# Kernel optimization log

Measured on AMD Instinct MI355X. Metric: run time of the kernel, lower is better.

## Reference

```python
import jax, jax.numpy as jnp
import numpy as np

B, T, C, H = 8, 2048, 1024, 128

def setup_inputs() -> dict:
    key = jax.random.key(0)
    k1, k2, k3, k4 = jax.random.split(key, 4)
    s = 1.0 / np.sqrt(C)
    return {
        "x": jax.random.normal(k1, (B, T, C), dtype=jnp.float32),
        "Wq": jax.random.normal(k2, (C, H), dtype=jnp.float32) * s,
        "Wk": jax.random.normal(k3, (C, H), dtype=jnp.float32) * s,
        "Wv": jax.random.normal(k4, (C, H), dtype=jnp.float32) * s,
    }

def reference(x, Wq, Wk, Wv):
    # q,k,v: [B,T,H]
    q = jnp.einsum('btc,ch->bth', x, Wq)
    k = jnp.einsum('btc,ch->bth', x, Wk)
    v = jnp.einsum('btc,ch->bth', x, Wv)
    scale = k.shape[-1] ** -0.5
    wei = jnp.einsum('bqh,bkh->bqk', q, k) * scale  # [B,T,T]
    # NOTE: original forward never applies the tril mask -> full bidirectional softmax
    wei = jax.nn.softmax(wei, axis=-1)
    # dropout p=0 (eval): identity
    out = jnp.einsum('bqk,bkh->bqh', wei, v)  # [B,T,H]
    return out
```

## Files before the change

kernel.cpp:

```cpp
#include <hip/hip_runtime.h>

typedef __attribute__((ext_vector_type(4))) float  f32x4;
typedef __attribute__((ext_vector_type(8))) short  s16x8;
typedef __attribute__((ext_vector_type(4))) unsigned int u32x4;
typedef __attribute__((ext_vector_type(4))) unsigned short u16x4;

#define NB 8
#define NT 2048
#define NC 1024
#define NH 128
#define NM (NB * NT)

__device__ __forceinline__ unsigned short f2bf(float f) {
  union { float f; unsigned u; } v; v.f = f;
  unsigned r = v.u + 0x7FFFu + ((v.u >> 16) & 1u);
  return (unsigned short)(r >> 16);
}
__device__ __forceinline__ unsigned pack2(float a, float b) {
  return (unsigned)f2bf(a) | ((unsigned)f2bf(b) << 16);
}
__device__ __forceinline__ f32x4 mfma16(s16x8 a, s16x8 b, f32x4 c) {
  return __builtin_amdgcn_mfma_f32_16x16x32_bf16(a, b, c, 0, 0, 0);
}

__global__ __launch_bounds__(256) void k_prep_w(
    const float* __restrict__ wq, const float* __restrict__ wk,
    const float* __restrict__ wv, unsigned short* __restrict__ wt3) {
  int id = blockIdx.x * 256 + threadIdx.x;
  int w = id >> 17;
  int r = id & 131071;
  int c = r & 1023;
  int h = r >> 10;
  const float* W = (w == 0) ? wq : (w == 1) ? wk : wv;
  float v = W[c * NH + h];
  if (w == 0) v *= 0.08838834764831845f;
  wt3[id] = f2bf(v);
}

__global__ __launch_bounds__(256, 2) void k_qkv(
    const float* __restrict__ x, const unsigned short* __restrict__ wt3,
    unsigned short* __restrict__ qo, unsigned short* __restrict__ ko,
    unsigned short* __restrict__ vo) {
  __shared__ u32x4 xs4[32 * 64 * 2 / 16];
  char* xs = (char*)xs4;
  const int tid = threadIdx.x;
  const int lane = tid & 63;
  const int w = tid >> 6;
  const int m0 = blockIdx.x * 32;

  const int sr = tid >> 3;
  const int scb = (tid & 7) * 16;
  const float* xp = x + (size_t)(m0 + sr) * NC + (tid & 7) * 8;
  const int wb = (sr * 128 + scb) ^ ((sr & 7) << 4);

  const int arow = lane & 15;
  const int aswz = (arow & 7) << 4;
  const int akb = (lane >> 4) * 16;
  const int n0 = w * 96;

  f32x4 acc[2][6] = {};
  f32x4 xa = *(const f32x4*)(xp);
  f32x4 xb = *(const f32x4*)(xp + 4);

  for (int kt = 0; kt < 16; ++kt) {
    __syncthreads();
    u32x4 pk = { pack2(xa.x, xa.y), pack2(xa.z, xa.w),
                 pack2(xb.x, xb.y), pack2(xb.z, xb.w) };
    *(u32x4*)(xs + wb) = pk;
    __syncthreads();
    if (kt < 15) {
      xa = *(const f32x4*)(xp + (kt + 1) * 64);
      xb = *(const f32x4*)(xp + (kt + 1) * 64 + 4);
    }
    #pragma unroll
    for (int ks = 0; ks < 2; ++ks) {
      s16x8 a0 = *(const s16x8*)(xs + (((arow)      * 128 + ks * 64 + akb) ^ aswz));
      s16x8 a1 = *(const s16x8*)(xs + (((arow + 16) * 128 + ks * 64 + akb) ^ aswz));
      const unsigned short* wp = wt3 + (size_t)(n0 + (lane & 15)) * NC
                                 + kt * 64 + ks * 32 + (lane >> 4) * 8;
      #pragma unroll
      for (int nj = 0; nj < 6; ++nj) {
        s16x8 bf = *(const s16x8*)(wp + (size_t)nj * 16 * NC);
        acc[0][nj] = mfma16(a0, bf, acc[0][nj]);
        acc[1][nj] = mfma16(a1, bf, acc[1][nj]);
      }
    }
  }
  const int rl = (lane >> 4) * 4;
  #pragma unroll
  for (int m = 0; m < 2; ++m) {
    #pragma unroll
    for (int nj = 0; nj < 6; ++nj) {
      f32x4 a = acc[m][nj];
      int gcol = n0 + nj * 16 + (lane & 15);
      int gr = m0 + m * 16 + rl;
      int h = gcol & 127;
      if (gcol < 256) {
        unsigned short* dst = (gcol < 128) ? qo : ko;
        dst[(size_t)(gr + 0) * NH + h] = f2bf(a.x);
        dst[(size_t)(gr + 1) * NH + h] = f2bf(a.y);
        dst[(size_t)(gr + 2) * NH + h] = f2bf(a.z);
        dst[(size_t)(gr + 3) * NH + h] = f2bf(a.w);
      } else {
        int bb = gr >> 11, tt = gr & 2047;
        u16x4 pv = { f2bf(a.x), f2bf(a.y), f2bf(a.z), f2bf(a.w) };
        *(u16x4*)(vo + ((size_t)(bb * NH + h) * NT + tt)) = pv;
      }
    }
  }
}

__global__ __launch_bounds__(256) void k_attn(
    const unsigned short* __restrict__ qg, const unsigned short* __restrict__ kg,
    const unsigned short* __restrict__ vg, float* __restrict__ out) {
  __shared__ u32x4 lds4[40 * 1024 / 16];
  char* Ks = (char*)lds4;
  char* Vs = Ks + 16 * 1024;
  char* Ps = Vs + 16 * 1024;
  const int tid = threadIdx.x;
  const int lane = tid & 63;
  const int w = tid >> 6;
  const int b = blockIdx.y;
  const int qr = blockIdx.x * 64 + w * 16;
  const int c15 = lane & 15;
  const int g4 = lane >> 4;

  s16x8 qf[4];
  #pragma unroll
  for (int ks = 0; ks < 4; ++ks)
    qf[ks] = *(const s16x8*)(qg + (size_t)(b * NT + qr + c15) * NH + ks * 32 + g4 * 8);

  float m_run[4], l_run[4];
  #pragma unroll
  for (int r = 0; r < 4; ++r) { m_run[r] = -3.0e38f; l_run[r] = 0.0f; }
  f32x4 acc_o[8] = {};

  const int skr = tid >> 4;
  const unsigned short* kbase = kg + (size_t)b * NT * NH + (tid & 15) * 8;
  const int svh = tid >> 3;
  const unsigned short* vbase = vg + (size_t)(b * NH) * NT + (tid & 7) * 8;

  u32x4 kreg[4], vreg[4];
  #pragma unroll
  for (int i = 0; i < 4; ++i) {
    kreg[i] = *(const u32x4*)(kbase + (size_t)(skr + i * 16) * NH);
    vreg[i] = *(const u32x4*)(vbase + (size_t)(svh + i * 32) * NT);
  }
  auto write_tiles = [&]() {
    #pragma unroll
    for (int i = 0; i < 4; ++i) {
      int r = skr + i * 16;
      *(u32x4*)(Ks + ((r * 256 + (tid & 15) * 16) ^ ((r & 7) << 4))) = kreg[i];
      int h = svh + i * 32;
      *(u32x4*)(Vs + ((h * 128 + (tid & 7) * 16) ^ ((h & 7) << 4))) = vreg[i];
    }
  };
  write_tiles();
  __syncthreads();

  char* pw = Ps + w * 2048;

  for (int kt = 0; kt < 32; ++kt) {
    if (kt < 31) {
      #pragma unroll
      for (int i = 0; i < 4; ++i) {
        kreg[i] = *(const u32x4*)(kbase + (size_t)((kt + 1) * 64 + skr + i * 16) * NH);
        vreg[i] = *(const u32x4*)(vbase + (size_t)(svh + i * 32) * NT + (kt + 1) * 64);
      }
    }
    f32x4 s[4] = {};
    #pragma unroll
    for (int nj = 0; nj < 4; ++nj) {
      int krow = nj * 16 + c15;
      int kswz = (krow & 7) << 4;
      #pragma unroll
      for (int ks = 0; ks < 4; ++ks) {
        s16x8 bf = *(const s16x8*)(Ks + ((krow * 256 + ks * 64 + g4 * 16) ^ kswz));
        s[nj] = mfma16(qf[ks], bf, s[nj]);
      }
    }
    float alpha[4];
    #pragma unroll
    for (int r = 0; r < 4; ++r) {
      float pm = fmaxf(fmaxf(s[0][r], s[1][r]), fmaxf(s[2][r], s[3][r]));
      pm = fmaxf(pm, __shfl_xor(pm, 1));
      pm = fmaxf(pm, __shfl_xor(pm, 2));
      pm = fmaxf(pm, __shfl_xor(pm, 4));
      pm = fmaxf(pm, __shfl_xor(pm, 8));
      float mn = fmaxf(m_run[r], pm);
      alpha[r] = __expf(m_run[r] - mn);
      m_run[r] = mn;
      float e0 = __expf(s[0][r] - mn);
      float e1 = __expf(s[1][r] - mn);
      float e2 = __expf(s[2][r] - mn);
      float e3 = __expf(s[3][r] - mn);
      s[0][r] = e0; s[1][r] = e1; s[2][r] = e2; s[3][r] = e3;
      float ps = e0 + e1 + e2 + e3;
      ps += __shfl_xor(ps, 1);
      ps += __shfl_xor(ps, 2);
      ps += __shfl_xor(ps, 4);
      ps += __shfl_xor(ps, 8);
      l_run[r] = l_run[r] * alpha[r] + ps;
    }
    #pragma unroll
    for (int hj = 0; hj < 8; ++hj) {
      acc_o[hj][0] *= alpha[0]; acc_o[hj][1] *= alpha[1];
      acc_o[hj][2] *= alpha[2]; acc_o[hj][3] *= alpha[3];
    }
    #pragma unroll
    for (int nj = 0; nj < 4; ++nj) {
      int colb = (nj * 16 + c15) * 2;
      #pragma unroll
      for (int r = 0; r < 4; ++r) {
        int row = g4 * 4 + r;
        *(unsigned short*)(pw + ((row * 128 + colb) ^ ((row & 7) << 4))) = f2bf(s[nj][r]);
      }
    }
    #pragma unroll
    for (int ks2 = 0; ks2 < 2; ++ks2) {
      s16x8 pa = *(const s16x8*)(pw + ((c15 * 128 + ks2 * 64 + g4 * 16) ^ ((c15 & 7) << 4)));
      #pragma unroll
      for (int hj = 0; hj < 8; ++hj) {
        int vrow = hj * 16 + c15;
        s16x8 bv = *(const s16x8*)(Vs + ((vrow * 128 + ks2 * 64 + g4 * 16) ^ ((vrow & 7) << 4)));
        acc_o[hj] = mfma16(pa, bv, acc_o[hj]);
      }
    }
    __syncthreads();
    if (kt < 31) write_tiles();
    __syncthreads();
  }
  float inv[4];
  #pragma unroll
  for (int r = 0; r < 4; ++r) inv[r] = 1.0f / l_run[r];
  #pragma unroll
  for (int hj = 0; hj < 8; ++hj) {
    int h = hj * 16 + c15;
    #pragma unroll
    for (int r = 0; r < 4; ++r) {
      int t = qr + g4 * 4 + r;
      out[(size_t)(b * NT + t) * NH + h] = acc_o[hj][r] * inv[r];
    }
  }
}

extern "C" void kernel_launch(void* const* d_in, const int* in_sizes, int n_in,
                              void* d_out, int out_size, void* d_ws, size_t ws_size,
                              hipStream_t stream) {
  const float* x  = (const float*)d_in[0];
  const float* wq = (const float*)d_in[1];
  const float* wk = (const float*)d_in[2];
  const float* wv = (const float*)d_in[3];
  unsigned short* ws  = (unsigned short*)d_ws;
  unsigned short* qb  = ws;
  unsigned short* kb  = ws + (size_t)2 * 1024 * 1024;
  unsigned short* vb  = ws + (size_t)4 * 1024 * 1024;
  unsigned short* wt3 = ws + (size_t)6 * 1024 * 1024;

  k_prep_w<<<dim3(1536), dim3(256), 0, stream>>>(wq, wk, wv, wt3);
  k_qkv<<<dim3(NM / 32), dim3(256), 0, stream>>>(x, wt3, qb, kb, vb);
  k_attn<<<dim3(NT / 64, NB), dim3(256), 0, stream>>>(qb, kb, vb, (float*)d_out);
}
```

Before: 219.0 us.

## Split attention KV across two wave groups, double-buffer tiles, tile weight transpose

The attention kernel now runs 512 threads per block. Two groups of four waves each process half of the key/value sequence, using double-buffered K/V tiles in LDS (144 KB) so each iteration needs one barrier instead of two. The two partial softmax states are merged through LDS at the end. The row-sum shuffle reduction is deferred to after the loop, and s_setprio wraps the MFMA sections. The QKV projection also moves to 64-row, 512-thread blocks with double-buffered x staging, and the weight transpose now goes through an LDS tile for coalesced reads and writes. The large LDS footprint limits occupancy to one block per CU, and the merge step adds an epilogue.

```diff
diff --git a/kernel.cpp b/kernel.cpp
--- a/kernel.cpp
+++ b/kernel.cpp
@@ -26,56 +26,71 @@
 __global__ __launch_bounds__(256) void k_prep_w(
     const float* __restrict__ wq, const float* __restrict__ wk,
     const float* __restrict__ wv, unsigned short* __restrict__ wt3) {
-  int id = blockIdx.x * 256 + threadIdx.x;
-  int w = id >> 17;
-  int r = id & 131071;
-  int c = r & 1023;
-  int h = r >> 10;
+  __shared__ float ts[64][65];
+  const int tid = threadIdx.x;
+  const int w = blockIdx.x >> 5;
+  const int rem = blockIdx.x & 31;
+  const int c0 = (rem >> 1) * 64;
+  const int h0 = (rem & 1) * 64;
   const float* W = (w == 0) ? wq : (w == 1) ? wk : wv;
-  float v = W[c * NH + h];
-  if (w == 0) v *= 0.08838834764831845f;
-  wt3[id] = f2bf(v);
-}
-
-__global__ __launch_bounds__(256, 2) void k_qkv(
+  const int hl = tid & 63, ci = tid >> 6;
+  #pragma unroll
+  for (int i = 0; i < 16; ++i) {
+    int cl = i * 4 + ci;
+    ts[cl][hl] = W[(size_t)(c0 + cl) * NH + h0 + hl];
+  }
+  __syncthreads();
+  const int cl2 = tid & 63, hi2 = tid >> 6;
+  #pragma unroll
+  for (int j = 0; j < 16; ++j) {
+    int hl2 = j * 4 + hi2;
+    float v = ts[cl2][hl2];
+    if (w == 0) v *= 0.08838834764831845f;
+    wt3[(size_t)w * 131072 + (size_t)(h0 + hl2) * NC + c0 + cl2] = f2bf(v);
+  }
+}
+
+__global__ __launch_bounds__(512) void k_qkv(
     const float* __restrict__ x, const unsigned short* __restrict__ wt3,
     unsigned short* __restrict__ qo, unsigned short* __restrict__ ko,
     unsigned short* __restrict__ vo) {
-  __shared__ u32x4 xs4[32 * 64 * 2 / 16];
+  __shared__ u32x4 xs4[2 * 64 * 128 / 16];
   char* xs = (char*)xs4;
   const int tid = threadIdx.x;
   const int lane = tid & 63;
   const int w = tid >> 6;
-  const int m0 = blockIdx.x * 32;
+  const int m0 = blockIdx.x * 64;
 
   const int sr = tid >> 3;
-  const int scb = (tid & 7) * 16;
   const float* xp = x + (size_t)(m0 + sr) * NC + (tid & 7) * 8;
-  const int wb = (sr * 128 + scb) ^ ((sr & 7) << 4);
-
-  const int arow = lane & 15;
-  const int aswz = (arow & 7) << 4;
+  const int wb = (sr * 128 + (tid & 7) * 16) ^ ((sr & 7) << 4);
+
+  const int mg = w >> 2;
+  const int n0 = (w & 3) * 96;
+  const int arow0 = mg * 32 + (lane & 15);
+  const int aswz = (arow0 & 7) << 4;
   const int akb = (lane >> 4) * 16;
-  const int n0 = w * 96;
 
   f32x4 acc[2][6] = {};
   f32x4 xa = *(const f32x4*)(xp);
   f32x4 xb = *(const f32x4*)(xp + 4);
-
-  for (int kt = 0; kt < 16; ++kt) {
-    __syncthreads();
+  {
     u32x4 pk = { pack2(xa.x, xa.y), pack2(xa.z, xa.w),
                  pack2(xb.x, xb.y), pack2(xb.z, xb.w) };
     *(u32x4*)(xs + wb) = pk;
-    __syncthreads();
+  }
+  __syncthreads();
+
+  for (int kt = 0; kt < 16; ++kt) {
     if (kt < 15) {
       xa = *(const f32x4*)(xp + (kt + 1) * 64);
       xb = *(const f32x4*)(xp + (kt + 1) * 64 + 4);
     }
+    char* cb = xs + (kt & 1) * 8192;
     #pragma unroll
     for (int ks = 0; ks < 2; ++ks) {
-      s16x8 a0 = *(const s16x8*)(xs + (((arow)      * 128 + ks * 64 + akb) ^ aswz));
-      s16x8 a1 = *(const s16x8*)(xs + (((arow + 16) * 128 + ks * 64 + akb) ^ aswz));
+      s16x8 a0 = *(const s16x8*)(cb + (((arow0)      * 128 + ks * 64 + akb) ^ aswz));
+      s16x8 a1 = *(const s16x8*)(cb + (((arow0 + 16) * 128 + ks * 64 + akb) ^ aswz));
       const unsigned short* wp = wt3 + (size_t)(n0 + (lane & 15)) * NC
                                  + kt * 64 + ks * 32 + (lane >> 4) * 8;
       #pragma unroll
@@ -85,6 +100,12 @@
         acc[1][nj] = mfma16(a1, bf, acc[1][nj]);
       }
     }
+    if (kt < 15) {
+      u32x4 pk = { pack2(xa.x, xa.y), pack2(xa.z, xa.w),
+                   pack2(xb.x, xb.y), pack2(xb.z, xb.w) };
+      *(u32x4*)(xs + ((kt + 1) & 1) * 8192 + wb) = pk;
+    }
+    __syncthreads();
   }
   const int rl = (lane >> 4) * 4;
   #pragma unroll
@@ -93,7 +114,7 @@
     for (int nj = 0; nj < 6; ++nj) {
       f32x4 a = acc[m][nj];
       int gcol = n0 + nj * 16 + (lane & 15);
-      int gr = m0 + m * 16 + rl;
+      int gr = m0 + mg * 32 + m * 16 + rl;
       int h = gcol & 127;
       if (gcol < 256) {
         unsigned short* dst = (gcol < 128) ? qo : ko;
@@ -110,35 +131,41 @@
   }
 }
 
-__global__ __launch_bounds__(256) void k_attn(
+__global__ __launch_bounds__(512) void k_attn(
     const unsigned short* __restrict__ qg, const unsigned short* __restrict__ kg,
     const unsigned short* __restrict__ vg, float* __restrict__ out) {
-  __shared__ u32x4 lds4[40 * 1024 / 16];
-  char* Ks = (char*)lds4;
-  char* Vs = Ks + 16 * 1024;
-  char* Ps = Vs + 16 * 1024;
+  __shared__ u32x4 lds4[147456 / 16];
+  char* L = (char*)lds4;
   const int tid = threadIdx.x;
   const int lane = tid & 63;
   const int w = tid >> 6;
+  const int grp = w >> 2;
+  const int wq = w & 3;
+  const int gt = tid & 255;
   const int b = blockIdx.y;
-  const int qr = blockIdx.x * 64 + w * 16;
+  const int qr = blockIdx.x * 64 + wq * 16;
   const int c15 = lane & 15;
   const int g4 = lane >> 4;
+  const int kv0 = grp * 1024;
+
+  char* Kb0 = L + grp * 65536;
+  char* Vb0 = L + grp * 65536 + 32768;
+  char* pw  = L + 131072 + w * 2048;
 
   s16x8 qf[4];
   #pragma unroll
   for (int ks = 0; ks < 4; ++ks)
     qf[ks] = *(const s16x8*)(qg + (size_t)(b * NT + qr + c15) * NH + ks * 32 + g4 * 8);
 
-  float m_run[4], l_run[4];
-  #pragma unroll
-  for (int r = 0; r < 4; ++r) { m_run[r] = -3.0e38f; l_run[r] = 0.0f; }
+  float m_run[4], lsum[4];
+  #pragma unroll
+  for (int r = 0; r < 4; ++r) { m_run[r] = -3.0e38f; lsum[r] = 0.0f; }
   f32x4 acc_o[8] = {};
 
-  const int skr = tid >> 4;
-  const unsigned short* kbase = kg + (size_t)b * NT * NH + (tid & 15) * 8;
-  const int svh = tid >> 3;
-  const unsigned short* vbase = vg + (size_t)(b * NH) * NT + (tid & 7) * 8;
+  const int skr = gt >> 4;
+  const unsigned short* kbase = kg + (size_t)(b * NT + kv0) * NH + (gt & 15) * 8;
+  const int svh = gt >> 3;
+  const unsigned short* vbase = vg + (size_t)(b * NH) * NT + kv0 + (gt & 7) * 8;
 
   u32x4 kreg[4], vreg[4];
   #pragma unroll
@@ -146,22 +173,22 @@
     kreg[i] = *(const u32x4*)(kbase + (size_t)(skr + i * 16) * NH);
     vreg[i] = *(const u32x4*)(vbase + (size_t)(svh + i * 32) * NT);
   }
-  auto write_tiles = [&]() {
+  auto write_tiles = [&](char* Kd, char* Vd) {
     #pragma unroll
     for (int i = 0; i < 4; ++i) {
       int r = skr + i * 16;
-      *(u32x4*)(Ks + ((r * 256 + (tid & 15) * 16) ^ ((r & 7) << 4))) = kreg[i];
+      *(u32x4*)(Kd + ((r * 256 + (gt & 15) * 16) ^ ((r & 7) << 4))) = kreg[i];
       int h = svh + i * 32;
-      *(u32x4*)(Vs + ((h * 128 + (tid & 7) * 16) ^ ((h & 7) << 4))) = vreg[i];
+      *(u32x4*)(Vd + ((h * 128 + (gt & 7) * 16) ^ ((h & 7) << 4))) = vreg[i];
     }
   };
-  write_tiles();
+  write_tiles(Kb0, Vb0);
   __syncthreads();
 
-  char* pw = Ps + w * 2048;
-
-  for (int kt = 0; kt < 32; ++kt) {
-    if (kt < 31) {
+  for (int kt = 0; kt < 16; ++kt) {
+    char* Ks = Kb0 + (kt & 1) * 16384;
+    char* Vs = Vb0 + (kt & 1) * 16384;
+    if (kt < 15) {
       #pragma unroll
       for (int i = 0; i < 4; ++i) {
         kreg[i] = *(const u32x4*)(kbase + (size_t)((kt + 1) * 64 + skr + i * 16) * NH);
@@ -169,6 +196,7 @@
       }
     }
     f32x4 s[4] = {};
+    __builtin_amdgcn_s_setprio(1);
     #pragma unroll
     for (int nj = 0; nj < 4; ++nj) {
       int krow = nj * 16 + c15;
@@ -179,6 +207,7 @@
         s[nj] = mfma16(qf[ks], bf, s[nj]);
       }
     }
+    __builtin_amdgcn_s_setprio(0);
     float alpha[4];
     #pragma unroll
     for (int r = 0; r < 4; ++r) {
@@ -195,12 +224,7 @@
       float e2 = __expf(s[2][r] - mn);
       float e3 = __expf(s[3][r] - mn);
       s[0][r] = e0; s[1][r] = e1; s[2][r] = e2; s[3][r] = e3;
-      float ps = e0 + e1 + e2 + e3;
-      ps += __shfl_xor(ps, 1);
-      ps += __shfl_xor(ps, 2);
-      ps += __shfl_xor(ps, 4);
-      ps += __shfl_xor(ps, 8);
-      l_run[r] = l_run[r] * alpha[r] + ps;
+      lsum[r] = lsum[r] * alpha[r] + (e0 + e1 + e2 + e3);
     }
     #pragma unroll
     for (int hj = 0; hj < 8; ++hj) {
@@ -216,6 +240,7 @@
         *(unsigned short*)(pw + ((row * 128 + colb) ^ ((row & 7) << 4))) = f2bf(s[nj][r]);
       }
     }
+    __builtin_amdgcn_s_setprio(1);
     #pragma unroll
     for (int ks2 = 0; ks2 < 2; ++ks2) {
       s16x8 pa = *(const s16x8*)(pw + ((c15 * 128 + ks2 * 64 + g4 * 16) ^ ((c15 & 7) << 4)));
@@ -226,20 +251,48 @@
         acc_o[hj] = mfma16(pa, bv, acc_o[hj]);
       }
     }
+    __builtin_amdgcn_s_setprio(0);
+    if (kt < 15) write_tiles(Kb0 + ((kt + 1) & 1) * 16384, Vb0 + ((kt + 1) & 1) * 16384);
     __syncthreads();
-    if (kt < 31) write_tiles();
-    __syncthreads();
-  }
-  float inv[4];
-  #pragma unroll
-  for (int r = 0; r < 4; ++r) inv[r] = 1.0f / l_run[r];
-  #pragma unroll
-  for (int hj = 0; hj < 8; ++hj) {
-    int h = hj * 16 + c15;
+  }
+  float l_run[4];
+  #pragma unroll
+  for (int r = 0; r < 4; ++r) {
+    float ls = lsum[r];
+    ls += __shfl_xor(ls, 1);
+    ls += __shfl_xor(ls, 2);
+    ls += __shfl_xor(ls, 4);
+    ls += __shfl_xor(ls, 8);
+    l_run[r] = ls;
+  }
+  float* msh = (float*)(L + 32768);
+  float* lsh = (float*)(L + 32768 + 256);
+  if (grp == 1) {
     #pragma unroll
     for (int r = 0; r < 4; ++r) {
-      int t = qr + g4 * 4 + r;
-      out[(size_t)(b * NT + t) * NH + h] = acc_o[hj][r] * inv[r];
+      int row = wq * 16 + g4 * 4 + r;
+      #pragma unroll
+      for (int hj = 0; hj < 8; ++hj)
+        *(float*)(L + ((row * 512 + (hj * 16 + c15) * 4) ^ ((row & 7) << 4))) = acc_o[hj][r];
+      if (c15 == 0) { msh[row] = m_run[r]; lsh[row] = l_run[r]; }
+    }
+  }
+  __syncthreads();
+  if (grp == 0) {
+    #pragma unroll
+    for (int r = 0; r < 4; ++r) {
+      int row = wq * 16 + g4 * 4 + r;
+      float m1 = msh[row], l1 = lsh[row];
+      float M = fmaxf(m_run[r], m1);
+      float w0 = __expf(m_run[r] - M);
+      float w1 = __expf(m1 - M);
+      float den = 1.0f / (w0 * l_run[r] + w1 * l1);
+      #pragma unroll
+      for (int hj = 0; hj < 8; ++hj) {
+        float o1 = *(const float*)(L + ((row * 512 + (hj * 16 + c15) * 4) ^ ((row & 7) << 4)));
+        out[(size_t)(b * NT + qr + g4 * 4 + r) * NH + hj * 16 + c15] =
+            (w0 * acc_o[hj][r] + w1 * o1) * den;
+      }
     }
   }
 }
@@ -257,7 +310,7 @@
   unsigned short* vb  = ws + (size_t)4 * 1024 * 1024;
   unsigned short* wt3 = ws + (size_t)6 * 1024 * 1024;
 
-  k_prep_w<<<dim3(1536), dim3(256), 0, stream>>>(wq, wk, wv, wt3);
-  k_qkv<<<dim3(NM / 32), dim3(256), 0, stream>>>(x, wt3, qb, kb, vb);
-  k_attn<<<dim3(NT / 64, NB), dim3(256), 0, stream>>>(qb, kb, vb, (float*)d_out);
-}
+  k_prep_w<<<dim3(96), dim3(256), 0, stream>>>(wq, wk, wv, wt3);
+  k_qkv<<<dim3(NM / 64), dim3(512), 0, stream>>>(x, wt3, qb, kb, vb);
+  k_attn<<<dim3(NT / 64, NB), dim3(512), 0, stream>>>(qb, kb, vb, (float*)d_out);
+}
```

New measurement: 189.3 us. 1.16x faster.
